# Kernel optimization log

Measured on AMD Instinct MI355X. Metric: run time of the kernel, lower is better.

## Reference

```python
import jax, jax.numpy as jnp
import numpy as np

B, S, D = 16, 1024, 1024

def _xavier_uniform(key, shape, fan_in, fan_out):
    a = float(np.sqrt(6.0 / (fan_in + fan_out)))
    return jax.random.uniform(key, shape, jnp.float32, -a, a)

def setup_inputs() -> dict:
    key = jax.random.key(0)
    ks = jax.random.split(key, 8)
    query = jax.random.normal(ks[0], (B, S, D), jnp.float32)
    key_t = jax.random.normal(ks[1], (B, S, D), jnp.float32)
    value = jax.random.normal(ks[2], (B, S, D), jnp.float32)
    # learned additive attention bias [1, S, S], xavier_uniform init
    attn_bias = _xavier_uniform(ks[3], (1, S, S), S, S)
    # Linear weights (torch nn.Linear default: kaiming-uniform-ish; any init ok for baseline)
    Wq = _xavier_uniform(ks[4], (D, D), D, D)
    bq = jnp.zeros((D,), jnp.float32)
    Wk = _xavier_uniform(ks[5], (D, D), D, D)
    bk = jnp.zeros((D,), jnp.float32)
    return {"query": query, "key": key_t, "value": value,
            "attn_bias": attn_bias, "Wq": Wq, "bq": bq, "Wk": Wk, "bk": bk}

def reference(query, key, value, attn_bias, Wq, bq, Wk, bk):
    # q = query @ Wq^T + bq  (torch Linear convention)
    q = jnp.einsum('bsd,ed->bse', query, Wq) + bq            # [B,S,D]
    k = jnp.einsum('bsd,ed->bse', key, Wk) + bk              # [B,S,D]
    energy = jnp.einsum('bsd,btd->bst', q, k) + attn_bias    # [B,S,S] (bias broadcasts over B)
    attention = jax.nn.softmax(energy, axis=-1)
    out = jnp.einsum('bst,btd->bsd', attention, value)       # value is NOT projected (matches source)
    return (out, attention)
```

## Files before the change

### kernel.cpp

```cpp
#include <hip/hip_runtime.h>


#define AS1 __attribute__((address_space(1)))
#define AS3 __attribute__((address_space(3)))
#define VMCNT(n) asm volatile("s_waitcnt vmcnt(" #n ")" ::: "memory")
#define LGKM(n)  asm volatile("s_waitcnt lgkmcnt(" #n ")" ::: "memory")
#define SBARRIER asm volatile("s_barrier" ::: "memory")
#define SB0 __builtin_amdgcn_sched_barrier(0)

typedef __bf16 bf16;
typedef __bf16 bf16x4 __attribute__((ext_vector_type(4)));
typedef __bf16 bf16x8 __attribute__((ext_vector_type(8)));
typedef float  f32x4  __attribute__((ext_vector_type(4)));
typedef float  f32x16 __attribute__((ext_vector_type(16)));

constexpr int BATCH = 16;
constexpr int S = 1024;
constexpr int D = 1024;
constexpr long NBSD = (long)BATCH * S * D;

constexpr int GBM = 256, GBN = 256, GBK = 32;
constexpr int NTK = 1024 / GBK;
constexpr int ARR = GBM * GBK;

__device__ __forceinline__ void stage16(const bf16* src, const bf16* dst) {
  __builtin_amdgcn_global_load_lds((const AS1 void*)src, (AS3 void*)dst, 16, 0, 0);
}

__global__ __launch_bounds__(256) void split_convert(
    const float* __restrict__ in, bf16* __restrict__ hi, bf16* __restrict__ lo, int n4) {
  int i = blockIdx.x * blockDim.x + threadIdx.x;
  int stride = gridDim.x * blockDim.x;
  for (; i < n4; i += stride) {
    f32x4 x = ((const f32x4*)in)[i];
    bf16x4 h, l;
#pragma unroll
    for (int j = 0; j < 4; ++j) {
      float v = x[j];
      bf16 hh = (bf16)v;
      h[j] = hh;
      l[j] = (bf16)(v - (float)hh);
    }
    ((bf16x4*)hi)[i] = h;
    ((bf16x4*)lo)[i] = l;
  }
}

__global__ __launch_bounds__(256) void transpose_convert(
    const float* __restrict__ v, bf16* __restrict__ vT) {
  __shared__ float tile[32][33];
  const int b = blockIdx.z;
  const int t0 = blockIdx.y * 32, d0 = blockIdx.x * 32;
  const int tx = threadIdx.x & 31, ty = threadIdx.x >> 5;
  const float* src = v + (long)b * S * D;
#pragma unroll
  for (int i = 0; i < 4; ++i)
    tile[ty + i * 8][tx] = src[(long)(t0 + ty + i * 8) * D + d0 + tx];
  __syncthreads();
  bf16* dst = vT + (long)b * D * S;
#pragma unroll
  for (int i = 0; i < 4; ++i)
    dst[(long)(d0 + ty + i * 8) * S + t0 + tx] = (bf16)tile[tx][ty + i * 8];
}

template <int EPI>
__global__ __launch_bounds__(512, 2) void gemm32_split(
    const bf16* __restrict__ Ah_g, const bf16* __restrict__ Al_g, long a_bs,
    const bf16* __restrict__ Bh_g, const bf16* __restrict__ Bl_g, long b_bs,
    const float* __restrict__ bias,
    bf16* __restrict__ Ch, bf16* __restrict__ Cl,
    float* __restrict__ Cf, long c_bs) {
  __shared__ bf16 lds[2 * 4 * ARR];

  const int tid = threadIdx.x;
  const int lane = tid & 63, wid = tid >> 6;
  const int wr = wid >> 2, wc = wid & 3;
  const int lr = lane & 31;
  const int lk = lane >> 5;

  const int w = blockIdx.x;
  const int swz = (w & 7) * 32 + (w >> 3);
  int z, by, bx;
  if constexpr (EPI == 0) { z = 0; by = swz >> 2; bx = swz & 3; }
  else { z = swz >> 4; by = (swz >> 2) & 3; bx = swz & 3; }
  const long brow = (long)by * GBM, bcol = (long)bx * GBN;

  const bf16* A_h = Ah_g + (long)z * a_bs;
  const bf16* A_l = Al_g + (long)z * a_bs;
  const bf16* B_h = Bh_g + (long)z * b_bs;
  const bf16* B_l = Bl_g + (long)z * b_bs;

  const int srow = tid >> 2;
  const int csw = ((tid & 3) ^ ((srow >> 1) & 3)) * 8;
  const long asrc = (brow + srow) * 1024 + csw;
  const long bsrc = (bcol + srow) * 1024 + csw;
  const int dstoff = wid * 512;

  int aoff[4][2], boff[2][2];
#pragma unroll
  for (int i = 0; i < 4; ++i) {
    const int r = wr * 128 + i * 32 + lr;
#pragma unroll
    for (int s = 0; s < 2; ++s)
      aoff[i][s] = r * 32 + (((2 * s + lk) ^ ((r >> 1) & 3)) * 8);
  }
#pragma unroll
  for (int j = 0; j < 2; ++j) {
    const int r = wc * 64 + j * 32 + lr;
#pragma unroll
    for (int s = 0; s < 2; ++s)
      boff[j][s] = r * 32 + (((2 * s + lk) ^ ((r >> 1) & 3)) * 8);
  }

  f32x16 acc[4][2] = {};
  bf16x8 ah[4][2], al[4][2], bh[2][2], bl[2][2];

#define STG(slot, arr, base, koff, rr) \
  stage16((base) + (koff) + (long)(rr) * 131072, \
          lds + ((slot) * 4 + (arr)) * ARR + (rr) * 4096 + dstoff)

#define CLUSTER(AF, BF) \
  __builtin_amdgcn_s_setprio(1); \
  _Pragma("unroll") \
  for (int s = 0; s < 2; ++s) \
    _Pragma("unroll") \
    for (int i = 0; i < 4; ++i) \
      _Pragma("unroll") \
      for (int j = 0; j < 2; ++j) \
        acc[i][j] = __builtin_amdgcn_mfma_f32_32x32x16_bf16(AF[i][s], BF[j][s], acc[i][j], 0, 0, 0); \
  __builtin_amdgcn_s_setprio(0)

  STG(0, 0, A_h + asrc, 0, 0); STG(0, 0, A_h + asrc, 0, 1);
  STG(0, 2, B_h + bsrc, 0, 0); STG(0, 2, B_h + bsrc, 0, 1);
  STG(0, 3, B_l + bsrc, 0, 0); STG(0, 3, B_l + bsrc, 0, 1);
  STG(0, 1, A_l + asrc, 0, 0); STG(0, 1, A_l + asrc, 0, 1);
  VMCNT(4);
  SBARRIER;

  for (int t = 0; t < NTK; ++t) {
    const int cur = t & 1, nxt = cur ^ 1;
    const long kn = (long)(t + 1) * GBK;
    const bool pf = (t + 1 < NTK);
    const bf16* lA_h = lds + (cur * 4 + 0) * ARR;
    const bf16* lA_l = lds + (cur * 4 + 1) * ARR;
    const bf16* lB_h = lds + (cur * 4 + 2) * ARR;
    const bf16* lB_l = lds + (cur * 4 + 3) * ARR;

#pragma unroll
    for (int i = 0; i < 4; ++i)
#pragma unroll
      for (int s = 0; s < 2; ++s) ah[i][s] = *(const bf16x8*)&lA_h[aoff[i][s]];
#pragma unroll
    for (int j = 0; j < 2; ++j)
#pragma unroll
      for (int s = 0; s < 2; ++s) bh[j][s] = *(const bf16x8*)&lB_h[boff[j][s]];
    if (pf) {
      STG(nxt, 0, A_h + asrc, kn, 0); STG(nxt, 0, A_h + asrc, kn, 1);
      STG(nxt, 2, B_h + bsrc, kn, 0); STG(nxt, 2, B_h + bsrc, kn, 1);
      VMCNT(6);
    } else {
      VMCNT(2);
    }
    SBARRIER; LGKM(0); SB0;
    CLUSTER(ah, bh);
    SBARRIER;

#pragma unroll
    for (int j = 0; j < 2; ++j)
#pragma unroll
      for (int s = 0; s < 2; ++s) bl[j][s] = *(const bf16x8*)&lB_l[boff[j][s]];
    if (pf) {
      STG(nxt, 3, B_l + bsrc, kn, 0); STG(nxt, 3, B_l + bsrc, kn, 1);
      VMCNT(6);
    } else {
      VMCNT(0);
    }
    SBARRIER; LGKM(0); SB0;
    CLUSTER(ah, bl);
    SBARRIER;

#pragma unroll
    for (int i = 0; i < 4; ++i)
#pragma unroll
      for (int s = 0; s < 2; ++s) al[i][s] = *(const bf16x8*)&lA_l[aoff[i][s]];
    if (pf) {
      STG(nxt, 1, A_l + asrc, kn, 0); STG(nxt, 1, A_l + asrc, kn, 1);
      VMCNT(4);
    }
    SBARRIER; LGKM(0); SB0;
    CLUSTER(al, bh);
    SBARRIER;
  }
#undef STG
#undef CLUSTER

  if constexpr (EPI == 0) {
#pragma unroll
    for (int j = 0; j < 2; ++j) {
      const long col = bcol + wc * 64 + j * 32 + lr;
      const float bv = bias[col];
#pragma unroll
      for (int i = 0; i < 4; ++i) {
        const long row0 = brow + wr * 128 + i * 32 + 4 * lk;
#pragma unroll
        for (int r = 0; r < 16; ++r) {
          const long row = row0 + (r & 3) + 8 * (r >> 2);
          const float c = acc[i][j][r] + bv;
          const bf16 h = (bf16)c;
          const bf16 l = (bf16)(c - (float)h);
          const long idx = row * 1024 + col;
          Ch[idx] = h;
          Cl[idx] = l;
        }
      }
    }
  } else {
    float* Cz = Cf + (long)z * c_bs;
#pragma unroll
    for (int j = 0; j < 2; ++j) {
      const long col = bcol + wc * 64 + j * 32 + lr;
#pragma unroll
      for (int i = 0; i < 4; ++i) {
        const long row0 = brow + wr * 128 + i * 32 + 4 * lk;
#pragma unroll
        for (int r = 0; r < 16; ++r) {
          const long row = row0 + (r & 3) + 8 * (r >> 2);
          Cz[row * 1024 + col] = acc[i][j][r] + bias[row * 1024 + col];
        }
      }
    }
  }
}

__global__ __launch_bounds__(512, 2) void gemm8_plain(
    const bf16* __restrict__ A_g, long a_bs,
    const bf16* __restrict__ B_g, long b_bs,
    float* __restrict__ C, long c_bs) {
  __shared__ bf16 lds[2 * 2 * ARR];

  const int tid = threadIdx.x;
  const int lane = tid & 63, wid = tid >> 6;
  const int wr = wid >> 2, wc = wid & 3;
  const int fr = lane & 15, fq = lane >> 4;
  const int fsw = (fr >> 1) & 3;

  const int w = blockIdx.x;
  const int swz = (w & 7) * 32 + (w >> 3);
  const int z = swz >> 4, by = (swz >> 2) & 3, bx = swz & 3;
  const long brow = (long)by * GBM, bcol = (long)bx * GBN;

  const bf16* A = A_g + (long)z * a_bs;
  const bf16* B = B_g + (long)z * b_bs;

  const int srow = tid >> 2;
  const int csw = ((tid & 3) ^ ((srow >> 1) & 3)) * 8;
  const long asrc = (brow + srow) * 1024 + csw;
  const long bsrc = (bcol + srow) * 1024 + csw;
  const int dstoff = wid * 512;

  const int aoffb = (wr * 128 + fr) * 32 + (fq ^ fsw) * 8;
  const int boffb = (wc * 64 + fr) * 32 + (fq ^ fsw) * 8;

  f32x4 acc[8][4] = {};

#define STG2(slot, arr, base, koff, rr) \
  stage16((base) + (koff) + (long)(rr) * 131072, \
          lds + ((slot) * 2 + (arr)) * ARR + (rr) * 4096 + dstoff)

  STG2(0, 0, A + asrc, 0, 0); STG2(0, 0, A + asrc, 0, 1);
  STG2(0, 1, B + bsrc, 0, 0); STG2(0, 1, B + bsrc, 0, 1);

  for (int t = 0; t < NTK; ++t) {
    const int cur = t & 1, nxt = cur ^ 1;
    const bf16* lA = lds + (cur * 2 + 0) * ARR;
    const bf16* lB = lds + (cur * 2 + 1) * ARR;

    if (t + 1 < NTK) {
      const long kn = (long)(t + 1) * GBK;
      STG2(nxt, 0, A + asrc, kn, 0); STG2(nxt, 0, A + asrc, kn, 1);
      STG2(nxt, 1, B + bsrc, kn, 0); STG2(nxt, 1, B + bsrc, kn, 1);
      VMCNT(4);
    } else {
      VMCNT(0);
    }
    SB0;
    SBARRIER;

    bf16x8 ah[8], bh[4];
#pragma unroll
    for (int m = 0; m < 8; ++m) ah[m] = *(const bf16x8*)&lA[aoffb + m * 512];
#pragma unroll
    for (int n = 0; n < 4; ++n) bh[n] = *(const bf16x8*)&lB[boffb + n * 512];
#pragma unroll
    for (int n = 0; n < 4; ++n)
#pragma unroll
      for (int m = 0; m < 8; ++m)
        acc[m][n] = __builtin_amdgcn_mfma_f32_16x16x32_bf16(ah[m], bh[n], acc[m][n], 0, 0, 0);

    SBARRIER;
  }
#undef STG2

  float* Cz = C + (long)z * c_bs;
#pragma unroll
  for (int n = 0; n < 4; ++n) {
    const long col = bcol + wc * 64 + n * 16 + fr;
#pragma unroll
    for (int m = 0; m < 8; ++m) {
      const long row0 = brow + wr * 128 + m * 16 + fq * 4;
#pragma unroll
      for (int j = 0; j < 4; ++j)
        Cz[(row0 + j) * 1024 + col] = acc[m][n][j];
    }
  }
}

__global__ __launch_bounds__(256) void softmax_rows(
    float* __restrict__ attn, bf16* __restrict__ attn_bf) {
  const long row = blockIdx.x;
  float* p = attn + row * 1024;
  const int tid = threadIdx.x, lane = tid & 63, wid = tid >> 6;

  f32x4 x = ((const f32x4*)p)[tid];
  float m = fmaxf(fmaxf(x[0], x[1]), fmaxf(x[2], x[3]));
#pragma unroll
  for (int off = 32; off; off >>= 1) m = fmaxf(m, __shfl_xor(m, off));
  __shared__ float redm[4];
  if (lane == 0) redm[wid] = m;
  __syncthreads();
  m = fmaxf(fmaxf(redm[0], redm[1]), fmaxf(redm[2], redm[3]));

  f32x4 e;
#pragma unroll
  for (int j = 0; j < 4; ++j) e[j] = __expf(x[j] - m);
  float s = e[0] + e[1] + e[2] + e[3];
#pragma unroll
  for (int off = 32; off; off >>= 1) s += __shfl_xor(s, off);
  __shared__ float reds[4];
  if (lane == 0) reds[wid] = s;
  __syncthreads();
  s = reds[0] + reds[1] + reds[2] + reds[3];

  const float inv = 1.0f / s;
  f32x4 r;
  bf16x4 rb;
#pragma unroll
  for (int j = 0; j < 4; ++j) {
    r[j] = e[j] * inv;
    rb[j] = (bf16)r[j];
  }
  ((f32x4*)p)[tid] = r;
  ((bf16x4*)(attn_bf + row * 1024))[tid] = rb;
}

extern "C" void kernel_launch(void* const* d_in, const int* in_sizes, int n_in,
                              void* d_out, int out_size, void* d_ws, size_t ws_size,
                              hipStream_t stream) {
  const float* query     = (const float*)d_in[0];
  const float* key       = (const float*)d_in[1];
  const float* value     = (const float*)d_in[2];
  const float* attn_bias = (const float*)d_in[3];
  const float* Wq        = (const float*)d_in[4];
  const float* bq        = (const float*)d_in[5];
  const float* Wk        = (const float*)d_in[6];
  const float* bk        = (const float*)d_in[7];

  float* out  = (float*)d_out;
  float* attn = out + NBSD;

  bf16* ws    = (bf16*)d_ws;
  bf16* q_hi  = ws;
  bf16* q_lo  = ws + NBSD;
  bf16* k_hi  = ws + 2 * NBSD;
  bf16* k_lo  = ws + 3 * NBSD;
  bf16* Wq_hi = ws + 4 * NBSD;
  bf16* Wq_lo = Wq_hi + (long)D * D;
  bf16* Wk_hi = Wq_lo + (long)D * D;
  bf16* Wk_lo = Wk_hi + (long)D * D;
  bf16* scr   = Wk_lo + (long)D * D;
  bf16* key_hi = scr;
  bf16* key_lo = scr + NBSD;
  bf16* valueT  = scr;
  bf16* attn_bf = scr + NBSD;
  bf16* query_hi = (bf16*)d_out;
  bf16* query_lo = query_hi + NBSD;

  split_convert<<<2048, 256, 0, stream>>>(query, query_hi, query_lo, (int)(NBSD / 4));
  split_convert<<<2048, 256, 0, stream>>>(key, key_hi, key_lo, (int)(NBSD / 4));
  split_convert<<<512, 256, 0, stream>>>(Wq, Wq_hi, Wq_lo, D * D / 4);
  split_convert<<<512, 256, 0, stream>>>(Wk, Wk_hi, Wk_lo, D * D / 4);

  gemm32_split<0><<<256, 512, 0, stream>>>(query_hi, query_lo, 0, Wq_hi, Wq_lo, 0,
                                           bq, q_hi, q_lo, nullptr, 0);
  gemm32_split<0><<<256, 512, 0, stream>>>(key_hi, key_lo, 0, Wk_hi, Wk_lo, 0,
                                           bk, k_hi, k_lo, nullptr, 0);

  transpose_convert<<<dim3(32, 32, 16), 256, 0, stream>>>(value, valueT);

  gemm32_split<1><<<256, 512, 0, stream>>>(q_hi, q_lo, (long)S * D, k_hi, k_lo, (long)S * D,
                                           attn_bias, nullptr, nullptr, attn, (long)S * S);

  softmax_rows<<<BATCH * S, 256, 0, stream>>>(attn, attn_bf);

  gemm8_plain<<<256, 512, 0, stream>>>(attn_bf, (long)S * S, valueT, (long)D * S,
                                       out, (long)S * D);
}
```

Measured before the change: 438.3 us.

## Software-pipeline LDS fragment reads with MFMA clusters in split-bf16 GEMM loop

Restructures the K loop of the bf16x3 split GEMM so LDS fragment loads for the next cluster are issued before the current MFMA cluster runs, using partial lgkmcnt waits instead of full drains. The high-part fragments for the next K tile are double-buffered in registers and loaded during the last cluster of the current tile. The loop is manually unrolled by two with the final tile peeled, and one barrier per stage is dropped. This aims to hide LDS latency behind MFMA work, at the cost of more registers, which may reduce occupancy or cause spills.

```diff
diff --git a/kernel.cpp b/kernel.cpp
--- a/kernel.cpp
+++ b/kernel.cpp
@@ -113,7 +113,7 @@
   }
 
   f32x16 acc[4][2] = {};
-  bf16x8 ah[4][2], al[4][2], bh[2][2], bl[2][2];
+  bf16x8 ahA[4][2], bhA[2][2], ahB[4][2], bhB[2][2], al[4][2], bl[2][2];
 
 #define STG(slot, arr, base, koff, rr) \
   stage16((base) + (koff) + (long)(rr) * 131072, \
@@ -130,69 +130,83 @@
         acc[i][j] = __builtin_amdgcn_mfma_f32_32x32x16_bf16(AF[i][s], BF[j][s], acc[i][j], 0, 0, 0); \
   __builtin_amdgcn_s_setprio(0)
 
+#define TILE_BODY(AH, BH, AHN, BHN, CUR, NXT, PF, KN) \
+  { \
+    const bf16* lA_l = lds + ((CUR) * 4 + 1) * ARR; \
+    const bf16* lB_l = lds + ((CUR) * 4 + 3) * ARR; \
+    const bf16* nA_h = lds + ((NXT) * 4 + 0) * ARR; \
+    const bf16* nB_h = lds + ((NXT) * 4 + 2) * ARR; \
+     \
+    if (PF) { \
+      STG(NXT, 0, A_h + asrc, KN, 0); STG(NXT, 0, A_h + asrc, KN, 1); \
+      STG(NXT, 2, B_h + bsrc, KN, 0); STG(NXT, 2, B_h + bsrc, KN, 1); \
+      VMCNT(6); \
+    } else { VMCNT(2); } \
+    SBARRIER; \
+    _Pragma("unroll") \
+    for (int j = 0; j < 2; ++j) \
+      _Pragma("unroll") \
+      for (int s = 0; s < 2; ++s) bl[j][s] = *(const bf16x8*)&lB_l[boff[j][s]]; \
+    LGKM(4); SB0; \
+    CLUSTER(AH, BH); \
+     \
+    if (PF) { STG(NXT, 3, B_l + bsrc, KN, 0); STG(NXT, 3, B_l + bsrc, KN, 1); VMCNT(6); } \
+    else { VMCNT(0); } \
+    SBARRIER; \
+    _Pragma("unroll") \
+    for (int i = 0; i < 4; ++i) \
+      _Pragma("unroll") \
+      for (int s = 0; s < 2; ++s) al[i][s] = *(const bf16x8*)&lA_l[aoff[i][s]]; \
+    LGKM(8); SB0; \
+    CLUSTER(AH, bl); \
+     \
+    if (PF) { STG(NXT, 1, A_l + asrc, KN, 0); STG(NXT, 1, A_l + asrc, KN, 1); VMCNT(4); } \
+    SBARRIER; \
+    if (PF) { \
+      _Pragma("unroll") \
+      for (int i = 0; i < 4; ++i) \
+        _Pragma("unroll") \
+        for (int s = 0; s < 2; ++s) AHN[i][s] = *(const bf16x8*)&nA_h[aoff[i][s]]; \
+      _Pragma("unroll") \
+      for (int j = 0; j < 2; ++j) \
+        _Pragma("unroll") \
+        for (int s = 0; s < 2; ++s) BHN[j][s] = *(const bf16x8*)&nB_h[boff[j][s]]; \
+      LGKM(12); \
+    } else { LGKM(0); } \
+    SB0; \
+    CLUSTER(al, BH); \
+  }
+
   STG(0, 0, A_h + asrc, 0, 0); STG(0, 0, A_h + asrc, 0, 1);
   STG(0, 2, B_h + bsrc, 0, 0); STG(0, 2, B_h + bsrc, 0, 1);
   STG(0, 3, B_l + bsrc, 0, 0); STG(0, 3, B_l + bsrc, 0, 1);
   STG(0, 1, A_l + asrc, 0, 0); STG(0, 1, A_l + asrc, 0, 1);
   VMCNT(4);
   SBARRIER;
-
-  for (int t = 0; t < NTK; ++t) {
-    const int cur = t & 1, nxt = cur ^ 1;
-    const long kn = (long)(t + 1) * GBK;
-    const bool pf = (t + 1 < NTK);
-    const bf16* lA_h = lds + (cur * 4 + 0) * ARR;
-    const bf16* lA_l = lds + (cur * 4 + 1) * ARR;
-    const bf16* lB_h = lds + (cur * 4 + 2) * ARR;
-    const bf16* lB_l = lds + (cur * 4 + 3) * ARR;
-
+  {
+    const bf16* lA_h0 = lds;
+    const bf16* lB_h0 = lds + 2 * ARR;
 #pragma unroll
     for (int i = 0; i < 4; ++i)
 #pragma unroll
-      for (int s = 0; s < 2; ++s) ah[i][s] = *(const bf16x8*)&lA_h[aoff[i][s]];
+      for (int s = 0; s < 2; ++s) ahA[i][s] = *(const bf16x8*)&lA_h0[aoff[i][s]];
 #pragma unroll
     for (int j = 0; j < 2; ++j)
 #pragma unroll
-      for (int s = 0; s < 2; ++s) bh[j][s] = *(const bf16x8*)&lB_h[boff[j][s]];
-    if (pf) {
-      STG(nxt, 0, A_h + asrc, kn, 0); STG(nxt, 0, A_h + asrc, kn, 1);
-      STG(nxt, 2, B_h + bsrc, kn, 0); STG(nxt, 2, B_h + bsrc, kn, 1);
-      VMCNT(6);
-    } else {
-      VMCNT(2);
-    }
-    SBARRIER; LGKM(0); SB0;
-    CLUSTER(ah, bh);
-    SBARRIER;
-
-#pragma unroll
-    for (int j = 0; j < 2; ++j)
-#pragma unroll
-      for (int s = 0; s < 2; ++s) bl[j][s] = *(const bf16x8*)&lB_l[boff[j][s]];
-    if (pf) {
-      STG(nxt, 3, B_l + bsrc, kn, 0); STG(nxt, 3, B_l + bsrc, kn, 1);
-      VMCNT(6);
-    } else {
-      VMCNT(0);
-    }
-    SBARRIER; LGKM(0); SB0;
-    CLUSTER(ah, bl);
-    SBARRIER;
-
-#pragma unroll
-    for (int i = 0; i < 4; ++i)
-#pragma unroll
-      for (int s = 0; s < 2; ++s) al[i][s] = *(const bf16x8*)&lA_l[aoff[i][s]];
-    if (pf) {
-      STG(nxt, 1, A_l + asrc, kn, 0); STG(nxt, 1, A_l + asrc, kn, 1);
-      VMCNT(4);
-    }
-    SBARRIER; LGKM(0); SB0;
-    CLUSTER(al, bh);
-    SBARRIER;
-  }
+      for (int s = 0; s < 2; ++s) bhA[j][s] = *(const bf16x8*)&lB_h0[boff[j][s]];
+  }
+
+  for (int tt = 0; tt < 15; ++tt) {
+    const long k1 = (long)(2 * tt + 1) * GBK;
+    const long k2 = (long)(2 * tt + 2) * GBK;
+    TILE_BODY(ahA, bhA, ahB, bhB, 0, 1, true, k1);
+    TILE_BODY(ahB, bhB, ahA, bhA, 1, 0, true, k2);
+  }
+  TILE_BODY(ahA, bhA, ahB, bhB, 0, 1, true, (long)31 * GBK);
+  TILE_BODY(ahB, bhB, ahA, bhA, 1, 0, false, 0);
 #undef STG
 #undef CLUSTER
+#undef TILE_BODY
 
   if constexpr (EPI == 0) {
 #pragma unroll
```

After: 478.1 us. 9.1% more time.

## Fold Wq and Wk into one combined matrix, dropping one projection GEMM

Applied to the files above, without the earlier changes.

Rewrites energy = (xWq^T+bq)(yWk^T+bk)^T as x·(Wq^T Wk)·y^T plus rank-1 bias terms. A small kernel precomputes the D×D product M^T = Wk^T Wq in fp32 and splits it into hi/lo bf16. The query is multiplied by this matrix, while key is only split-converted, never projected. The bias corrections (query·(Wq^T bk), key·(Wk^T bq), bq·bk) are computed in fused convert+dot kernels and added in the energy epilogue. This removes one of the two large projection GEMMs at the cost of extra small kernels and different rounding behaviour.

```diff
diff --git a/kernel.cpp b/kernel.cpp
--- a/kernel.cpp
+++ b/kernel.cpp
@@ -27,22 +27,123 @@
   __builtin_amdgcn_global_load_lds((const AS1 void*)src, (AS3 void*)dst, 16, 0, 0);
 }
 
-__global__ __launch_bounds__(256) void split_convert(
-    const float* __restrict__ in, bf16* __restrict__ hi, bf16* __restrict__ lo, int n4) {
-  int i = blockIdx.x * blockDim.x + threadIdx.x;
-  int stride = gridDim.x * blockDim.x;
-  for (; i < n4; i += stride) {
-    f32x4 x = ((const f32x4*)in)[i];
+__global__ __launch_bounds__(256) void split_convert_dot(
+    const float* __restrict__ in, bf16* __restrict__ hi, bf16* __restrict__ lo,
+    const float* __restrict__ w, float* __restrict__ v) {
+  const int wid = threadIdx.x >> 6, lane = threadIdx.x & 63;
+  const long row = (long)blockIdx.x * 4 + wid;
+  const f32x4* src = (const f32x4*)(in + row * 1024);
+  const f32x4* w4 = (const f32x4*)w;
+  float acc = 0.f;
+#pragma unroll
+  for (int it = 0; it < 4; ++it) {
+    const int idx = it * 64 + lane;
+    f32x4 x = src[idx];
+    f32x4 wv = w4[idx];
     bf16x4 h, l;
 #pragma unroll
     for (int j = 0; j < 4; ++j) {
-      float v = x[j];
-      bf16 hh = (bf16)v;
+      float vv = x[j];
+      bf16 hh = (bf16)vv;
       h[j] = hh;
-      l[j] = (bf16)(v - (float)hh);
-    }
-    ((bf16x4*)hi)[i] = h;
-    ((bf16x4*)lo)[i] = l;
+      l[j] = (bf16)(vv - (float)hh);
+      acc += vv * wv[j];
+    }
+    *(bf16x4*)(hi + row * 1024 + idx * 4) = h;
+    *(bf16x4*)(lo + row * 1024 + idx * 4) = l;
+  }
+#pragma unroll
+  for (int off = 32; off; off >>= 1) acc += __shfl_xor(acc, off);
+  if (lane == 0) v[row] = acc;
+}
+
+__global__ __launch_bounds__(256) void wpart_kernel(
+    const float* __restrict__ Wq, const float* __restrict__ Wk,
+    const float* __restrict__ bq, const float* __restrict__ bk,
+    float* __restrict__ w1p, float* __restrict__ w2p,
+    float* __restrict__ cbuf, float* __restrict__ zeros) {
+  const int b = blockIdx.x, t = threadIdx.x;
+  if (b < 32) {
+    const int dc = b >> 2, e = (b & 3) * 256 + t;
+    float s = 0.f;
+    for (int d = dc * 128; d < dc * 128 + 128; ++d) s += Wq[(long)d * 1024 + e] * bk[d];
+    w1p[dc * 1024 + e] = s;
+  } else if (b < 64) {
+    const int dc = (b - 32) >> 2, e = ((b - 32) & 3) * 256 + t;
+    float s = 0.f;
+    for (int d = dc * 128; d < dc * 128 + 128; ++d) s += Wk[(long)d * 1024 + e] * bq[d];
+    w2p[dc * 1024 + e] = s;
+  } else {
+    for (int i = t; i < 1024; i += 256) zeros[i] = 0.f;
+    float s = 0.f;
+    for (int i = t; i < 1024; i += 256) s += bq[i] * bk[i];
+#pragma unroll
+    for (int off = 32; off; off >>= 1) s += __shfl_xor(s, off);
+    __shared__ float red[4];
+    if ((t & 63) == 0) red[t >> 6] = s;
+    __syncthreads();
+    if (t == 0) cbuf[0] = red[0] + red[1] + red[2] + red[3];
+  }
+}
+
+__global__ __launch_bounds__(256) void wreduce_kernel(
+    const float* __restrict__ w1p, const float* __restrict__ w2p,
+    float* __restrict__ w1, float* __restrict__ w2) {
+  const int b = blockIdx.x, t = threadIdx.x;
+  if (b < 4) {
+    const int e = b * 256 + t;
+    float s = 0.f;
+#pragma unroll
+    for (int dc = 0; dc < 8; ++dc) s += w1p[dc * 1024 + e];
+    w1[e] = s;
+  } else {
+    const int e = (b - 4) * 256 + t;
+    float s = 0.f;
+#pragma unroll
+    for (int dc = 0; dc < 8; ++dc) s += w2p[dc * 1024 + e];
+    w2[e] = s;
+  }
+}
+
+__global__ __launch_bounds__(256) void mt_split(
+    const float* __restrict__ Wk, const float* __restrict__ Wq,
+    bf16* __restrict__ MTh, bf16* __restrict__ MTl) {
+  __shared__ float sK[64][64], sQ[64][64];
+  const int t = threadIdx.x;
+  const int j0 = blockIdx.y * 64, d0 = blockIdx.x * 64;
+  const int tj = t >> 4, td = t & 15;
+  float acc[4][4] = {};
+  for (int e0 = 0; e0 < 1024; e0 += 64) {
+    __syncthreads();
+#pragma unroll
+    for (int it = 0; it < 4; ++it) {
+      const int r = (t >> 4) + it * 16, c4 = (t & 15) * 4;
+      *(f32x4*)&sK[r][c4] = *(const f32x4*)&Wk[(long)(e0 + r) * 1024 + j0 + c4];
+      *(f32x4*)&sQ[r][c4] = *(const f32x4*)&Wq[(long)(e0 + r) * 1024 + d0 + c4];
+    }
+    __syncthreads();
+#pragma unroll 4
+    for (int e = 0; e < 64; ++e) {
+      f32x4 a = *(const f32x4*)&sK[e][tj * 4];
+      f32x4 b = *(const f32x4*)&sQ[e][td * 4];
+#pragma unroll
+      for (int i = 0; i < 4; ++i)
+#pragma unroll
+        for (int j = 0; j < 4; ++j)
+          acc[i][j] += a[i] * b[j];
+    }
+  }
+#pragma unroll
+  for (int i = 0; i < 4; ++i) {
+    const long row = j0 + tj * 4 + i;
+#pragma unroll
+    for (int j = 0; j < 4; ++j) {
+      const float c = acc[i][j];
+      const bf16 h = (bf16)c;
+      const long idx = row * 1024 + d0 + td * 4 + j;
+      MTh[idx] = h;
+      MTl[idx] = (bf16)(c - (float)h);
+    }
   }
 }
 
@@ -69,7 +170,9 @@
     const bf16* __restrict__ Bh_g, const bf16* __restrict__ Bl_g, long b_bs,
     const float* __restrict__ bias,
     bf16* __restrict__ Ch, bf16* __restrict__ Cl,
-    float* __restrict__ Cf, long c_bs) {
+    float* __restrict__ Cf, long c_bs,
+    const float* __restrict__ v1, const float* __restrict__ v2,
+    const float* __restrict__ cvec) {
   __shared__ bf16 lds[2 * 4 * ARR];
 
   const int tid = threadIdx.x;
@@ -216,16 +319,20 @@
     }
   } else {
     float* Cz = Cf + (long)z * c_bs;
+    const float cc = cvec[0];
+    const float* vz1 = v1 + (long)z * 1024;
+    const float* vz2 = v2 + (long)z * 1024;
 #pragma unroll
     for (int j = 0; j < 2; ++j) {
       const long col = bcol + wc * 64 + j * 32 + lr;
+      const float v2c = vz2[col] + cc;
 #pragma unroll
       for (int i = 0; i < 4; ++i) {
         const long row0 = brow + wr * 128 + i * 32 + 4 * lk;
 #pragma unroll
         for (int r = 0; r < 16; ++r) {
           const long row = row0 + (r & 3) + 8 * (r >> 2);
-          Cz[row * 1024 + col] = acc[i][j][r] + bias[row * 1024 + col];
+          Cz[row * 1024 + col] = acc[i][j][r] + bias[row * 1024 + col] + vz1[row] + v2c;
         }
       }
     }
@@ -368,37 +475,46 @@
   float* out  = (float*)d_out;
   float* attn = out + NBSD;
 
-  bf16* ws    = (bf16*)d_ws;
-  bf16* q_hi  = ws;
-  bf16* q_lo  = ws + NBSD;
-  bf16* k_hi  = ws + 2 * NBSD;
-  bf16* k_lo  = ws + 3 * NBSD;
-  bf16* Wq_hi = ws + 4 * NBSD;
-  bf16* Wq_lo = Wq_hi + (long)D * D;
-  bf16* Wk_hi = Wq_lo + (long)D * D;
-  bf16* Wk_lo = Wk_hi + (long)D * D;
-  bf16* scr   = Wk_lo + (long)D * D;
-  bf16* key_hi = scr;
-  bf16* key_lo = scr + NBSD;
-  bf16* valueT  = scr;
-  bf16* attn_bf = scr + NBSD;
-  bf16* query_hi = (bf16*)d_out;
-  bf16* query_lo = query_hi + NBSD;
-
-  split_convert<<<2048, 256, 0, stream>>>(query, query_hi, query_lo, (int)(NBSD / 4));
-  split_convert<<<2048, 256, 0, stream>>>(key, key_hi, key_lo, (int)(NBSD / 4));
-  split_convert<<<512, 256, 0, stream>>>(Wq, Wq_hi, Wq_lo, D * D / 4);
-  split_convert<<<512, 256, 0, stream>>>(Wk, Wk_hi, Wk_lo, D * D / 4);
-
-  gemm32_split<0><<<256, 512, 0, stream>>>(query_hi, query_lo, 0, Wq_hi, Wq_lo, 0,
-                                           bq, q_hi, q_lo, nullptr, 0);
-  gemm32_split<0><<<256, 512, 0, stream>>>(key_hi, key_lo, 0, Wk_hi, Wk_lo, 0,
-                                           bk, k_hi, k_lo, nullptr, 0);
+  bf16* ws      = (bf16*)d_ws;
+  bf16* k_hi    = ws;
+  bf16* k_lo    = ws + NBSD;
+  bf16* qm_hi   = ws + 2 * NBSD;
+  bf16* qm_lo   = ws + 3 * NBSD;
+  bf16* valueT  = ws + 4 * NBSD;
+  bf16* attn_bf = ws + 5 * NBSD;
+  bf16* smallb  = ws + 6 * NBSD;
+  bf16* MT_hi   = smallb;
+  bf16* MT_lo   = smallb + 1048576;
+  float* fsm    = (float*)(smallb + 2097152);
+  float* zeros  = fsm;
+  float* w1     = fsm + 1024;
+  float* w2     = fsm + 2048;
+  float* cbuf   = fsm + 3072;
+  float* v1     = fsm + 4096;
+  float* v2     = fsm + 20480;
+  float* w1p    = fsm + 36864;
+  float* w2p    = fsm + 45056;
+  bf16* q_hi = (bf16*)attn;
+  bf16* q_lo = q_hi + NBSD;
+
+  wpart_kernel<<<65, 256, 0, stream>>>(Wq, Wk, bq, bk, w1p, w2p, cbuf, zeros);
+  wreduce_kernel<<<8, 256, 0, stream>>>(w1p, w2p, w1, w2);
+
+  split_convert_dot<<<4096, 256, 0, stream>>>(query, q_hi, q_lo, w1, v1);
+  split_convert_dot<<<4096, 256, 0, stream>>>(key, k_hi, k_lo, w2, v2);
+
+  mt_split<<<dim3(16, 16), 256, 0, stream>>>(Wk, Wq, MT_hi, MT_lo);
+
+  gemm32_split<0><<<256, 512, 0, stream>>>(q_hi, q_lo, 0, MT_hi, MT_lo, 0,
+                                           zeros, qm_hi, qm_lo, nullptr, 0,
+                                           nullptr, nullptr, nullptr);
 
   transpose_convert<<<dim3(32, 32, 16), 256, 0, stream>>>(value, valueT);
 
-  gemm32_split<1><<<256, 512, 0, stream>>>(q_hi, q_lo, (long)S * D, k_hi, k_lo, (long)S * D,
-                                           attn_bias, nullptr, nullptr, attn, (long)S * S);
+  gemm32_split<1><<<256, 512, 0, stream>>>(qm_hi, qm_lo, (long)S * D,
+                                           k_hi, k_lo, (long)S * D,
+                                           attn_bias, nullptr, nullptr, attn, (long)S * S,
+                                           v1, v2, cbuf);
 
   softmax_rows<<<BATCH * S, 256, 0, stream>>>(attn, attn_bf);
 
```

Result: slower. 467.3 us (+6.6%).
